# Kernel optimization log

Measured on AMD Instinct MI355X. Metric: run time of the kernel, lower is better.

Reference implementation:

```python
import jax, jax.numpy as jnp
import numpy as np

H_S = 1024
N_HEADS = 16
P_S = H_S // N_HEADS
LN_EPS = 1e-5


def layer_norm(x, gamma, beta):
    mu = jnp.mean(x, axis=-1, keepdims=True)
    var = jnp.var(x, axis=-1, keepdims=True)
    return (x - mu) * jax.lax.rsqrt(var + LN_EPS) * gamma + beta


def setup_inputs() -> dict:
    key = jax.random.key(0)
    ks = jax.random.split(key, 8)
    scale = 1.0 / np.sqrt(H_S)
    B, S = 4, 2048
    return {
        "q": jax.random.normal(ks[0], (B, S, H_S), jnp.float32),
        "k": jax.random.normal(ks[1], (B, S, H_S), jnp.float32),
        "v": jax.random.normal(ks[2], (B, S, H_S), jnp.float32),
        "ln_q_g": jnp.ones((H_S,), jnp.float32),
        "ln_q_b": jnp.zeros((H_S,), jnp.float32),
        "ln_k_g": jnp.ones((H_S,), jnp.float32),
        "ln_k_b": jnp.zeros((H_S,), jnp.float32),
        "ln_v_g": jnp.ones((H_S,), jnp.float32),
        "ln_v_b": jnp.zeros((H_S,), jnp.float32),
        "w_q": jax.random.normal(ks[3], (H_S, H_S), jnp.float32) * scale,
        "w_k": jax.random.normal(ks[4], (H_S, H_S), jnp.float32) * scale,
        "w_v": jax.random.normal(ks[5], (H_S, H_S), jnp.float32) * scale,
        "w_fc": jax.random.normal(ks[6], (H_S, H_S), jnp.float32) * scale,
        "b_fc": jnp.zeros((H_S,), jnp.float32),
    }


def _split_heads(x):
    # (b, s, h_s) -> (b, n_heads, s, p_s)
    b, s, _ = x.shape
    return x.reshape(b, s, N_HEADS, P_S).transpose(0, 2, 1, 3)


def reference(q, k, v, ln_q_g, ln_q_b, ln_k_g, ln_k_b, ln_v_g, ln_v_b,
              w_q, w_k, w_v, w_fc, b_fc):
    b, q_l, _ = q.shape
    # LayerNorm + Linear (bias=False) for Q/K/V, then head split
    qh = _split_heads(layer_norm(q, ln_q_g, ln_q_b) @ w_q.T)
    kh = _split_heads(layer_norm(k, ln_k_g, ln_k_b) @ w_k.T)
    vh = _split_heads(layer_norm(v, ln_v_g, ln_v_b) @ w_v.T)
    # scaled dot-product attention (clipping_distance=None path), scale 1/sqrt(p_s)
    scores = jnp.einsum("bhqp,bhkp->bhqk", qh, kh) / jnp.sqrt(jnp.float32(P_S))
    attn = jax.nn.softmax(scores, axis=-1)
    ctx = jnp.einsum("bhqk,bhkp->bhqp", attn, vh)
    # join heads: (b, h, q, p) -> (b, q, h_s)
    ctx = ctx.transpose(0, 2, 1, 3).reshape(b, q_l, H_S)
    out = ctx @ w_fc.T + b_fc
    # residual (dropout p=0.0 -> identity)
    return q + out
```

## Files before the change

kernel.cpp:

```cpp
#include <hip/hip_runtime.h>

#define HS 1024
#define NH 16
#define PS 64
#define SS 2048
#define NB 4
#define MTOT (NB * SS)
#define QSCALE 0.18033688011112042f

typedef __bf16 bf16x8 __attribute__((ext_vector_type(8)));
typedef float f32x4 __attribute__((ext_vector_type(4)));

__device__ __forceinline__ unsigned short f2bf(float f) {
  union { __bf16 h; unsigned short u; } c;
  c.h = (__bf16)f;
  return c.u;
}
__device__ __forceinline__ unsigned int pk2(float a, float b) {
  union { __bf16 h[2]; unsigned int u; } c;
  c.h[0] = (__bf16)a; c.h[1] = (__bf16)b;
  return c.u;
}
__device__ __forceinline__ float exp2x(float x) {
  float r; asm("v_exp_f32 %0, %1" : "=v"(r) : "v"(x)); return r;
}
__device__ __forceinline__ int kp32(int k) {
  return (k & ~31) | ((k & 12) << 1) | ((k & 16) >> 2) | (k & 3);
}

__device__ __forceinline__ void gload16(const void* g, void* lds) {
  __builtin_amdgcn_global_load_lds(
      (const __attribute__((address_space(1))) unsigned int*)g,
      (__attribute__((address_space(3))) unsigned int*)lds, 16, 0, 0);
}

__device__ __forceinline__ bf16x8 ldfrag128(const unsigned short* base, int r, int c) {
  union { bf16x8 v; uint4 u; } f;
  f.u = *reinterpret_cast<const uint4*>(base + r * 64 + ((c ^ (r & 7)) << 3));
  return f.v;
}

__global__ __launch_bounds__(256) void ln3_kernel(
    const float* __restrict__ x0, const float* __restrict__ x1, const float* __restrict__ x2,
    const float* __restrict__ g0, const float* __restrict__ b0,
    const float* __restrict__ g1, const float* __restrict__ b1,
    const float* __restrict__ g2, const float* __restrict__ b2,
    unsigned short* __restrict__ y0, unsigned short* __restrict__ y1,
    unsigned short* __restrict__ y2) {
  const int z = blockIdx.y;
  const float* x = z == 0 ? x0 : z == 1 ? x1 : x2;
  const float* g = z == 0 ? g0 : z == 1 ? g1 : g2;
  const float* bt = z == 0 ? b0 : z == 1 ? b1 : b2;
  unsigned short* y = z == 0 ? y0 : z == 1 ? y1 : y2;
  const int row = blockIdx.x;
  const int t = threadIdx.x;
  const float4 v = reinterpret_cast<const float4*>(x + (size_t)row * HS)[t];
  float s = v.x + v.y + v.z + v.w;
  float s2 = v.x * v.x + v.y * v.y + v.z * v.z + v.w * v.w;
#pragma unroll
  for (int m = 32; m; m >>= 1) { s += __shfl_xor(s, m); s2 += __shfl_xor(s2, m); }
  __shared__ float red[8];
  if ((t & 63) == 0) { red[t >> 6] = s; red[4 + (t >> 6)] = s2; }
  __syncthreads();
  s = red[0] + red[1] + red[2] + red[3];
  s2 = red[4] + red[5] + red[6] + red[7];
  const float mean = s * (1.0f / HS);
  const float var = s2 * (1.0f / HS) - mean * mean;
  const float rs = rsqrtf(var + 1e-5f);
  const float4 gv = reinterpret_cast<const float4*>(g)[t];
  const float4 bv = reinterpret_cast<const float4*>(bt)[t];
  uint2 o;
  o.x = pk2((v.x - mean) * rs * gv.x + bv.x, (v.y - mean) * rs * gv.y + bv.y);
  o.y = pk2((v.z - mean) * rs * gv.z + bv.z, (v.w - mean) * rs * gv.w + bv.w);
  *reinterpret_cast<uint2*>(y + (size_t)row * HS + kp32(4 * t)) = o;
}

__global__ __launch_bounds__(256) void castw_kernel(
    const float* __restrict__ w0, const float* __restrict__ w1,
    const float* __restrict__ w2, const float* __restrict__ w3,
    unsigned short* __restrict__ o0, unsigned short* __restrict__ o1,
    unsigned short* __restrict__ o2, unsigned short* __restrict__ o3) {
  const int which = blockIdx.x >> 10;
  const float* w = which == 0 ? w0 : which == 1 ? w1 : which == 2 ? w2 : w3;
  unsigned short* o = which == 0 ? o0 : which == 1 ? o1 : which == 2 ? o2 : o3;
  const int i = (blockIdx.x & 1023) * 256 + threadIdx.x;
  float4 v = reinterpret_cast<const float4*>(w)[i];
  uint2 u;
  u.x = pk2(v.x, v.y);
  u.y = pk2(v.z, v.w);
  *reinterpret_cast<uint2*>(o + (size_t)(i >> 8) * 1024 + kp32((i << 2) & 1023)) = u;
}

__global__ __launch_bounds__(512, 4) void gemm_qkv(
    const unsigned short* __restrict__ Aq, const unsigned short* __restrict__ Ak,
    const unsigned short* __restrict__ Av, const unsigned short* __restrict__ Wq,
    const unsigned short* __restrict__ Wk, const unsigned short* __restrict__ Wv,
    unsigned short* __restrict__ Pq, unsigned short* __restrict__ Pk,
    unsigned short* __restrict__ Pv, int zbase) {
  const int z = zbase + blockIdx.z;
  const unsigned short* A = z == 0 ? Aq : z == 1 ? Ak : Av;
  const unsigned short* Bw = z == 0 ? Wq : z == 1 ? Wk : Wv;
  unsigned short* out = z == 0 ? Pq : z == 1 ? Pk : Pv;
  __shared__ unsigned short As[128 * 64];
  __shared__ unsigned short Bs[128 * 64];
  const int t = threadIdx.x;
  const int id = blockIdx.x + 8 * blockIdx.y;
  const int xcd = id & 7, j = id >> 3;
  const int colT = (j & 7) * 128;
  const int rowT = (xcd * 8 + (j >> 3)) * 128;
  const int lane = t & 63;
  const int w = t >> 6;
  const int wr = (w >> 2) * 64, wc = (w & 3) * 32;
  const int c16 = lane & 15, g = lane >> 4, g4 = g << 2;
  const unsigned short* Ab = A + (size_t)rowT * 1024;
  const unsigned short* Bb = Bw + (size_t)colT * 1024;
  f32x4 acc[4][2] = {};
  for (int kt = 0; kt < 1024; kt += 64) {
#pragma unroll
    for (int i = 0; i < 2; ++i) {
      const int c = i * 512 + t;
      const int col = kt + (((c ^ (c >> 3)) & 7) << 3);
      gload16(Ab + (size_t)(c >> 3) * 1024 + col, As + c * 8);
      gload16(Bb + (size_t)(c >> 3) * 1024 + col, Bs + c * 8);
    }
    __syncthreads();
#pragma unroll
    for (int kk = 0; kk < 2; ++kk) {
      bf16x8 aF[4], bF[2];
#pragma unroll
      for (int m = 0; m < 4; ++m) aF[m] = ldfrag128(As, wr + m * 16 + c16, kk * 4 + g);
#pragma unroll
      for (int n = 0; n < 2; ++n) bF[n] = ldfrag128(Bs, wc + n * 16 + c16, kk * 4 + g);
      __builtin_amdgcn_s_setprio(1);
#pragma unroll
      for (int m = 0; m < 4; ++m)
#pragma unroll
        for (int n = 0; n < 2; ++n)
          acc[m][n] = __builtin_amdgcn_mfma_f32_16x16x32_bf16(aF[m], bF[n], acc[m][n], 0, 0, 0);
      __builtin_amdgcn_s_setprio(0);
    }
    __syncthreads();
  }
  const float sc = (z == 0) ? QSCALE : 1.0f;
#pragma unroll
  for (int m = 0; m < 4; ++m) {
#pragma unroll
    for (int n = 0; n < 2; ++n) {
#pragma unroll
      for (int r = 0; r < 4; ++r) {
        const int row = rowT + wr + m * 16 + g4 + r;
        const int col = colT + wc + n * 16 + c16;
        const float val = acc[m][n][r] * sc;
        const int b = row >> 11, s = row & 2047, h = col >> 6, p = col & 63;
        if (z == 2) {
          out[(((size_t)(b * NH + h)) * PS + p) * SS + kp32(s)] = f2bf(val);
        } else {
          out[(((size_t)(b * NH + h)) * SS + s) * PS + kp32(p)] = f2bf(val);
        }
      }
    }
  }
}

__global__ __launch_bounds__(512, 4) void gemm_fc(
    const unsigned short* __restrict__ A, const unsigned short* __restrict__ Bw,
    float* __restrict__ out, const float* __restrict__ resid,
    const float* __restrict__ bias) {
  __shared__ unsigned short As[128 * 64];
  __shared__ unsigned short Bs[128 * 64];
  const int t = threadIdx.x;
  const int id = blockIdx.x + 8 * blockIdx.y;
  const int xcd = id & 7, j = id >> 3;
  const int colT = (j & 7) * 128;
  const int rowT = (xcd * 8 + (j >> 3)) * 128;
  const int lane = t & 63;
  const int w = t >> 6;
  const int wr = (w >> 2) * 64, wc = (w & 3) * 32;
  const int c16 = lane & 15, g = lane >> 4, g4 = g << 2;
  const unsigned short* Ab = A + (size_t)rowT * 1024;
  const unsigned short* Bb = Bw + (size_t)colT * 1024;
  f32x4 acc[4][2] = {};
  for (int kt = 0; kt < 1024; kt += 64) {
#pragma unroll
    for (int i = 0; i < 2; ++i) {
      const int c = i * 512 + t;
      const int col = kt + (((c ^ (c >> 3)) & 7) << 3);
      gload16(Ab + (size_t)(c >> 3) * 1024 + col, As + c * 8);
      gload16(Bb + (size_t)(c >> 3) * 1024 + col, Bs + c * 8);
    }
    __syncthreads();
#pragma unroll
    for (int kk = 0; kk < 2; ++kk) {
      bf16x8 aF[4], bF[2];
#pragma unroll
      for (int m = 0; m < 4; ++m) aF[m] = ldfrag128(As, wr + m * 16 + c16, kk * 4 + g);
#pragma unroll
      for (int n = 0; n < 2; ++n) bF[n] = ldfrag128(Bs, wc + n * 16 + c16, kk * 4 + g);
      __builtin_amdgcn_s_setprio(1);
#pragma unroll
      for (int m = 0; m < 4; ++m)
#pragma unroll
        for (int n = 0; n < 2; ++n)
          acc[m][n] = __builtin_amdgcn_mfma_f32_16x16x32_bf16(aF[m], bF[n], acc[m][n], 0, 0, 0);
      __builtin_amdgcn_s_setprio(0);
    }
    __syncthreads();
  }
#pragma unroll
  for (int m = 0; m < 4; ++m) {
#pragma unroll
    for (int n = 0; n < 2; ++n) {
#pragma unroll
      for (int r = 0; r < 4; ++r) {
        const int row = rowT + wr + m * 16 + g4 + r;
        const int col = colT + wc + n * 16 + c16;
        out[(size_t)row * HS + col] =
            acc[m][n][r] + bias[col] + resid[(size_t)row * HS + col];
      }
    }
  }
}

__device__ __forceinline__ void stage_kv(const unsigned short* Kb, const unsigned short* Vb,
                                         int tile, unsigned short* kd, unsigned short* vd,
                                         int t) {
  const int r = t >> 3;
  const int cc = ((t ^ r) & 7) << 3;
  gload16(Kb + (size_t)(tile * 64 + r) * PS + cc, kd + t * 8);
  gload16(Vb + (size_t)r * SS + tile * 64 + cc, vd + t * 8);
}

__global__ __launch_bounds__(512, 4) void attn_kernel(
    const unsigned short* __restrict__ Qp, const unsigned short* __restrict__ Kp,
    const unsigned short* __restrict__ Vtg, unsigned short* __restrict__ ctx) {
  __shared__ unsigned short Ks[3][64 * 64];
  __shared__ unsigned short Vs[3][64 * 64];
  const int t = threadIdx.x;
  const int w = t >> 6, lane = t & 63;
  const int c16 = lane & 15, g = lane >> 4, g4 = g << 2;
  const int id = blockIdx.x + 8 * blockIdx.y;
  const int xcd = id & 7, j = id >> 3;
  const int bh = xcd * 8 + (j >> 3);
  const int qbase = (j & 7) * 256 + w * 32;
  const unsigned short* Qb = Qp + (size_t)bh * SS * PS;
  const unsigned short* Kb = Kp + (size_t)bh * SS * PS;
  const unsigned short* Vb = Vtg + (size_t)bh * SS * PS;

  union { bf16x8 v; unsigned short s[8]; } ou;
#pragma unroll
  for (int i = 0; i < 8; ++i) ou.s[i] = 0x3F80;
  const bf16x8 onesv = ou.v;

  bf16x8 qF0[2], qF1[2];
#pragma unroll
  for (int kkc = 0; kkc < 2; ++kkc) {
    union { bf16x8 v; uint4 u; } f0, f1;
    f0.u = *reinterpret_cast<const uint4*>(Qb + (size_t)(qbase + c16) * PS + ((kkc * 4 + g) << 3));
    f1.u = *reinterpret_cast<const uint4*>(Qb + (size_t)(qbase + 16 + c16) * PS + ((kkc * 4 + g) << 3));
    qF0[kkc] = f0.v; qF1[kkc] = f1.v;
  }
  f32x4 o0[4] = {}, o1[4] = {};
  f32x4 ol0 = {}, ol1 = {};

  unsigned short *k0 = Ks[0], *k1 = Ks[1], *k2 = Ks[2];
  unsigned short *v0 = Vs[0], *v1 = Vs[1], *v2 = Vs[2];
  stage_kv(Kb, Vb, 0, k0, v0, t);
  stage_kv(Kb, Vb, 1, k1, v1, t);

  for (int kt = 0; kt < 32; ++kt) {
    if (kt < 30) {
      asm volatile("s_waitcnt vmcnt(2) lgkmcnt(0)" ::: "memory");
    } else {
      asm volatile("s_waitcnt vmcnt(0) lgkmcnt(0)" ::: "memory");
    }
    __builtin_amdgcn_s_barrier();
    __builtin_amdgcn_sched_barrier(0);
    if (kt + 2 < 32) stage_kv(Kb, Vb, kt + 2, k2, v2, t);

    f32x4 s0[4] = {}, s1[4] = {};
    __builtin_amdgcn_s_setprio(1);
#pragma unroll
    for (int kkc = 0; kkc < 2; ++kkc)
#pragma unroll
      for (int nf = 0; nf < 4; ++nf) {
        const bf16x8 kf = ldfrag128(k0, nf * 16 + c16, kkc * 4 + g);
        s0[nf] = __builtin_amdgcn_mfma_f32_16x16x32_bf16(kf, qF0[kkc], s0[nf], 0, 0, 0);
        s1[nf] = __builtin_amdgcn_mfma_f32_16x16x32_bf16(kf, qF1[kkc], s1[nf], 0, 0, 0);
      }
    __builtin_amdgcn_s_setprio(0);

#pragma unroll
    for (int nf = 0; nf < 4; ++nf)
#pragma unroll
      for (int r = 0; r < 4; ++r) {
        s0[nf][r] = exp2x(s0[nf][r]);
        s1[nf][r] = exp2x(s1[nf][r]);
      }

    __builtin_amdgcn_s_setprio(1);
#pragma unroll
    for (int kkc = 0; kkc < 2; ++kkc) {
      union { bf16x8 v; unsigned int u[4]; } pa0, pa1;
      pa0.u[0] = pk2(s0[2 * kkc][0], s0[2 * kkc][1]);
      pa0.u[1] = pk2(s0[2 * kkc][2], s0[2 * kkc][3]);
      pa0.u[2] = pk2(s0[2 * kkc + 1][0], s0[2 * kkc + 1][1]);
      pa0.u[3] = pk2(s0[2 * kkc + 1][2], s0[2 * kkc + 1][3]);
      pa1.u[0] = pk2(s1[2 * kkc][0], s1[2 * kkc][1]);
      pa1.u[1] = pk2(s1[2 * kkc][2], s1[2 * kkc][3]);
      pa1.u[2] = pk2(s1[2 * kkc + 1][0], s1[2 * kkc + 1][1]);
      pa1.u[3] = pk2(s1[2 * kkc + 1][2], s1[2 * kkc + 1][3]);
      ol0 = __builtin_amdgcn_mfma_f32_16x16x32_bf16(pa0.v, onesv, ol0, 0, 0, 0);
      ol1 = __builtin_amdgcn_mfma_f32_16x16x32_bf16(pa1.v, onesv, ol1, 0, 0, 0);
#pragma unroll
      for (int pf = 0; pf < 4; ++pf) {
        const bf16x8 vf = ldfrag128(v0, pf * 16 + c16, kkc * 4 + g);
        o0[pf] = __builtin_amdgcn_mfma_f32_16x16x32_bf16(pa0.v, vf, o0[pf], 0, 0, 0);
        o1[pf] = __builtin_amdgcn_mfma_f32_16x16x32_bf16(pa1.v, vf, o1[pf], 0, 0, 0);
      }
    }
    __builtin_amdgcn_s_setprio(0);

    unsigned short* tk = k0; k0 = k1; k1 = k2; k2 = tk;
    unsigned short* tv = v0; v0 = v1; v1 = v2; v2 = tv;
  }

  float i0[4], i1[4];
#pragma unroll
  for (int r = 0; r < 4; ++r) { i0[r] = 1.0f / ol0[r]; i1[r] = 1.0f / ol1[r]; }
  const int b = bh >> 4, h = bh & 15;
#pragma unroll
  for (int pf = 0; pf < 4; ++pf) {
#pragma unroll
    for (int r = 0; r < 4; ++r) {
      const int col = kp32(h * PS + pf * 16 + c16);
      const int sA = qbase + g4 + r, sB = qbase + 16 + g4 + r;
      ctx[((size_t)(b * SS + sA)) * HS + col] = f2bf(o0[pf][r] * i0[r]);
      ctx[((size_t)(b * SS + sB)) * HS + col] = f2bf(o1[pf][r] * i1[r]);
    }
  }
}

extern "C" void kernel_launch(void* const* d_in, const int* in_sizes, int n_in,
                              void* d_out, int out_size, void* d_ws, size_t ws_size,
                              hipStream_t stream) {
  const float* q = (const float*)d_in[0];
  const float* k = (const float*)d_in[1];
  const float* v = (const float*)d_in[2];
  const float* ln_q_g = (const float*)d_in[3];
  const float* ln_q_b = (const float*)d_in[4];
  const float* ln_k_g = (const float*)d_in[5];
  const float* ln_k_b = (const float*)d_in[6];
  const float* ln_v_g = (const float*)d_in[7];
  const float* ln_v_b = (const float*)d_in[8];
  const float* w_q = (const float*)d_in[9];
  const float* w_k = (const float*)d_in[10];
  const float* w_v = (const float*)d_in[11];
  const float* w_fc = (const float*)d_in[12];
  const float* b_fc = (const float*)d_in[13];

  char* ws = (char*)d_ws;
  const bool merged = ws_size >= ((size_t)104 << 20);

  if (merged) {
    unsigned short* xq = (unsigned short*)(ws);
    unsigned short* xk = (unsigned short*)(ws + (16 << 20));
    unsigned short* xv = (unsigned short*)(ws + (32 << 20));
    unsigned short* ctx = (unsigned short*)(ws);
    unsigned short* wqb = (unsigned short*)(ws + (48 << 20));
    unsigned short* wkb = (unsigned short*)(ws + (50 << 20));
    unsigned short* wvb = (unsigned short*)(ws + (52 << 20));
    unsigned short* wfcb = (unsigned short*)(ws + (54 << 20));
    unsigned short* pq = (unsigned short*)(ws + (56 << 20));
    unsigned short* pk = (unsigned short*)(ws + (72 << 20));
    unsigned short* pv = (unsigned short*)(ws + (88 << 20));

    castw_kernel<<<4096, 256, 0, stream>>>(w_q, w_k, w_v, w_fc, wqb, wkb, wvb, wfcb);
    ln3_kernel<<<dim3(MTOT, 3), 256, 0, stream>>>(q, k, v, ln_q_g, ln_q_b, ln_k_g,
                                                  ln_k_b, ln_v_g, ln_v_b, xq, xk, xv);
    gemm_qkv<<<dim3(8, 64, 3), 512, 0, stream>>>(xq, xk, xv, wqb, wkb, wvb, pq, pk, pv, 0);
    attn_kernel<<<dim3(8, 64), 512, 0, stream>>>(pq, pk, pv, ctx);
    gemm_fc<<<dim3(8, 64), 512, 0, stream>>>(ctx, wfcb, (float*)d_out, q, b_fc);
  } else {
    unsigned short* xln = (unsigned short*)(ws);
    unsigned short* ctx = (unsigned short*)(ws);
    unsigned short* wqb = (unsigned short*)(ws + (16 << 20));
    unsigned short* wkb = (unsigned short*)(ws + (18 << 20));
    unsigned short* wvb = (unsigned short*)(ws + (20 << 20));
    unsigned short* wfcb = (unsigned short*)(ws + (22 << 20));
    unsigned short* pq = (unsigned short*)(ws + (24 << 20));
    unsigned short* pk = (unsigned short*)(ws + (40 << 20));
    unsigned short* pv = (unsigned short*)(ws + (56 << 20));

    castw_kernel<<<4096, 256, 0, stream>>>(w_q, w_k, w_v, w_fc, wqb, wkb, wvb, wfcb);
    ln3_kernel<<<dim3(MTOT, 1), 256, 0, stream>>>(q, q, q, ln_q_g, ln_q_b, ln_q_g,
                                                  ln_q_b, ln_q_g, ln_q_b, xln, xln, xln);
    gemm_qkv<<<dim3(8, 64, 1), 512, 0, stream>>>(xln, xln, xln, wqb, wqb, wqb,
                                                 pq, pq, pq, 0);
    ln3_kernel<<<dim3(MTOT, 1), 256, 0, stream>>>(k, k, k, ln_k_g, ln_k_b, ln_k_g,
                                                  ln_k_b, ln_k_g, ln_k_b, xln, xln, xln);
    gemm_qkv<<<dim3(8, 64, 1), 512, 0, stream>>>(xln, xln, xln, wkb, wkb, wkb,
                                                 pk, pk, pk, 1);
    ln3_kernel<<<dim3(MTOT, 1), 256, 0, stream>>>(v, v, v, ln_v_g, ln_v_b, ln_v_g,
                                                  ln_v_b, ln_v_g, ln_v_b, xln, xln, xln);
    gemm_qkv<<<dim3(8, 64, 1), 512, 0, stream>>>(xln, xln, xln, wvb, wvb, wvb,
                                                 pv, pv, pv, 2);
    attn_kernel<<<dim3(8, 64), 512, 0, stream>>>(pq, pk, pv, ctx);
    gemm_fc<<<dim3(8, 64), 512, 0, stream>>>(ctx, wfcb, (float*)d_out, q, b_fc);
  }
}
```

Baseline: 204.5 us.

## Switch attention KV staging to 128-key double-buffered tiles

Replaces the triple-buffered 64-key K/V pipeline with a double-buffered pipeline that stages 128 keys per step, and processes each staged tile as two 64-key halves. This halves the number of barriers and waitcnt synchronisations per block. In exchange the prefetch distance drops from two tiles to one, each step waits for all outstanding loads (vmcnt(0)), and LDS use grows from 48KB to 64KB per block, which may limit occupancy.

After: 201.1 us. No clear change (-1.6%).

```diff
diff --git a/kernel.cpp b/kernel.cpp
--- a/kernel.cpp
+++ b/kernel.cpp
@@ -221,20 +221,28 @@
   }
 }
 
-__device__ __forceinline__ void stage_kv(const unsigned short* Kb, const unsigned short* Vb,
-                                         int tile, unsigned short* kd, unsigned short* vd,
-                                         int t) {
-  const int r = t >> 3;
-  const int cc = ((t ^ r) & 7) << 3;
-  gload16(Kb + (size_t)(tile * 64 + r) * PS + cc, kd + t * 8);
-  gload16(Vb + (size_t)r * SS + tile * 64 + cc, vd + t * 8);
+__device__ __forceinline__ void stage_kv128(const unsigned short* Kb,
+                                            const unsigned short* Vb, int tile,
+                                            unsigned short* kd, unsigned short* vd,
+                                            int t) {
+#pragma unroll
+  for (int i = 0; i < 2; ++i) {
+    const int c = i * 512 + t;
+    const int rk = c >> 3;
+    const int ck = ((c ^ rk) & 7) << 3;
+    gload16(Kb + (size_t)(tile * 128 + rk) * PS + ck, kd + c * 8);
+    const int cc = c & 511;
+    const int rv = cc >> 3;
+    const int cv = ((cc ^ rv) & 7) << 3;
+    gload16(Vb + (size_t)rv * SS + tile * 128 + i * 64 + cv, vd + c * 8);
+  }
 }
 
 __global__ __launch_bounds__(512, 4) void attn_kernel(
     const unsigned short* __restrict__ Qp, const unsigned short* __restrict__ Kp,
     const unsigned short* __restrict__ Vtg, unsigned short* __restrict__ ctx) {
-  __shared__ unsigned short Ks[3][64 * 64];
-  __shared__ unsigned short Vs[3][64 * 64];
+  __shared__ unsigned short Ks[2][128 * 64];
+  __shared__ unsigned short Vs[2][128 * 64];
   const int t = threadIdx.x;
   const int w = t >> 6, lane = t & 63;
   const int c16 = lane & 15, g = lane >> 4, g4 = g << 2;
@@ -262,66 +270,65 @@
   f32x4 o0[4] = {}, o1[4] = {};
   f32x4 ol0 = {}, ol1 = {};
 
-  unsigned short *k0 = Ks[0], *k1 = Ks[1], *k2 = Ks[2];
-  unsigned short *v0 = Vs[0], *v1 = Vs[1], *v2 = Vs[2];
-  stage_kv(Kb, Vb, 0, k0, v0, t);
-  stage_kv(Kb, Vb, 1, k1, v1, t);
-
-  for (int kt = 0; kt < 32; ++kt) {
-    if (kt < 30) {
-      asm volatile("s_waitcnt vmcnt(2) lgkmcnt(0)" ::: "memory");
-    } else {
-      asm volatile("s_waitcnt vmcnt(0) lgkmcnt(0)" ::: "memory");
-    }
+  stage_kv128(Kb, Vb, 0, Ks[0], Vs[0], t);
+
+  int buf = 0;
+  for (int kt = 0; kt < 16; ++kt) {
+    asm volatile("s_waitcnt vmcnt(0) lgkmcnt(0)" ::: "memory");
     __builtin_amdgcn_s_barrier();
     __builtin_amdgcn_sched_barrier(0);
-    if (kt + 2 < 32) stage_kv(Kb, Vb, kt + 2, k2, v2, t);
-
-    f32x4 s0[4] = {}, s1[4] = {};
-    __builtin_amdgcn_s_setprio(1);
-#pragma unroll
-    for (int kkc = 0; kkc < 2; ++kkc)
-#pragma unroll
-      for (int nf = 0; nf < 4; ++nf) {
-        const bf16x8 kf = ldfrag128(k0, nf * 16 + c16, kkc * 4 + g);
-        s0[nf] = __builtin_amdgcn_mfma_f32_16x16x32_bf16(kf, qF0[kkc], s0[nf], 0, 0, 0);
-        s1[nf] = __builtin_amdgcn_mfma_f32_16x16x32_bf16(kf, qF1[kkc], s1[nf], 0, 0, 0);
+    if (kt + 1 < 16) stage_kv128(Kb, Vb, kt + 1, Ks[buf ^ 1], Vs[buf ^ 1], t);
+
+#pragma unroll
+    for (int hh = 0; hh < 2; ++hh) {
+      const unsigned short* kh = &Ks[buf][hh * 4096];
+      const unsigned short* vh = &Vs[buf][hh * 4096];
+
+      f32x4 s0[4] = {}, s1[4] = {};
+      __builtin_amdgcn_s_setprio(1);
+#pragma unroll
+      for (int kkc = 0; kkc < 2; ++kkc)
+#pragma unroll
+        for (int nf = 0; nf < 4; ++nf) {
+          const bf16x8 kf = ldfrag128(kh, nf * 16 + c16, kkc * 4 + g);
+          s0[nf] = __builtin_amdgcn_mfma_f32_16x16x32_bf16(kf, qF0[kkc], s0[nf], 0, 0, 0);
+          s1[nf] = __builtin_amdgcn_mfma_f32_16x16x32_bf16(kf, qF1[kkc], s1[nf], 0, 0, 0);
+        }
+      __builtin_amdgcn_s_setprio(0);
+
+#pragma unroll
+      for (int nf = 0; nf < 4; ++nf)
+#pragma unroll
+        for (int r = 0; r < 4; ++r) {
+          s0[nf][r] = exp2x(s0[nf][r]);
+          s1[nf][r] = exp2x(s1[nf][r]);
+        }
+
+      __builtin_amdgcn_s_setprio(1);
+#pragma unroll
+      for (int kkc = 0; kkc < 2; ++kkc) {
+        union { bf16x8 v; unsigned int u[4]; } pa0, pa1;
+        pa0.u[0] = pk2(s0[2 * kkc][0], s0[2 * kkc][1]);
+        pa0.u[1] = pk2(s0[2 * kkc][2], s0[2 * kkc][3]);
+        pa0.u[2] = pk2(s0[2 * kkc + 1][0], s0[2 * kkc + 1][1]);
+        pa0.u[3] = pk2(s0[2 * kkc + 1][2], s0[2 * kkc + 1][3]);
+        pa1.u[0] = pk2(s1[2 * kkc][0], s1[2 * kkc][1]);
+        pa1.u[1] = pk2(s1[2 * kkc][2], s1[2 * kkc][3]);
+        pa1.u[2] = pk2(s1[2 * kkc + 1][0], s1[2 * kkc + 1][1]);
+        pa1.u[3] = pk2(s1[2 * kkc + 1][2], s1[2 * kkc + 1][3]);
+        ol0 = __builtin_amdgcn_mfma_f32_16x16x32_bf16(pa0.v, onesv, ol0, 0, 0, 0);
+        ol1 = __builtin_amdgcn_mfma_f32_16x16x32_bf16(pa1.v, onesv, ol1, 0, 0, 0);
+#pragma unroll
+        for (int pf = 0; pf < 4; ++pf) {
+          const bf16x8 vf = ldfrag128(vh, pf * 16 + c16, kkc * 4 + g);
+          o0[pf] = __builtin_amdgcn_mfma_f32_16x16x32_bf16(pa0.v, vf, o0[pf], 0, 0, 0);
+          o1[pf] = __builtin_amdgcn_mfma_f32_16x16x32_bf16(pa1.v, vf, o1[pf], 0, 0, 0);
+        }
       }
-    __builtin_amdgcn_s_setprio(0);
-
-#pragma unroll
-    for (int nf = 0; nf < 4; ++nf)
-#pragma unroll
-      for (int r = 0; r < 4; ++r) {
-        s0[nf][r] = exp2x(s0[nf][r]);
-        s1[nf][r] = exp2x(s1[nf][r]);
-      }
-
-    __builtin_amdgcn_s_setprio(1);
-#pragma unroll
-    for (int kkc = 0; kkc < 2; ++kkc) {
-      union { bf16x8 v; unsigned int u[4]; } pa0, pa1;
-      pa0.u[0] = pk2(s0[2 * kkc][0], s0[2 * kkc][1]);
-      pa0.u[1] = pk2(s0[2 * kkc][2], s0[2 * kkc][3]);
-      pa0.u[2] = pk2(s0[2 * kkc + 1][0], s0[2 * kkc + 1][1]);
-      pa0.u[3] = pk2(s0[2 * kkc + 1][2], s0[2 * kkc + 1][3]);
-      pa1.u[0] = pk2(s1[2 * kkc][0], s1[2 * kkc][1]);
-      pa1.u[1] = pk2(s1[2 * kkc][2], s1[2 * kkc][3]);
-      pa1.u[2] = pk2(s1[2 * kkc + 1][0], s1[2 * kkc + 1][1]);
-      pa1.u[3] = pk2(s1[2 * kkc + 1][2], s1[2 * kkc + 1][3]);
-      ol0 = __builtin_amdgcn_mfma_f32_16x16x32_bf16(pa0.v, onesv, ol0, 0, 0, 0);
-      ol1 = __builtin_amdgcn_mfma_f32_16x16x32_bf16(pa1.v, onesv, ol1, 0, 0, 0);
-#pragma unroll
-      for (int pf = 0; pf < 4; ++pf) {
-        const bf16x8 vf = ldfrag128(v0, pf * 16 + c16, kkc * 4 + g);
-        o0[pf] = __builtin_amdgcn_mfma_f32_16x16x32_bf16(pa0.v, vf, o0[pf], 0, 0, 0);
-        o1[pf] = __builtin_amdgcn_mfma_f32_16x16x32_bf16(pa1.v, vf, o1[pf], 0, 0, 0);
-      }
-    }
-    __builtin_amdgcn_s_setprio(0);
-
-    unsigned short* tk = k0; k0 = k1; k1 = k2; k2 = tk;
-    unsigned short* tv = v0; v0 = v1; v1 = v2; v2 = tv;
+      __builtin_amdgcn_s_setprio(0);
+    }
+
+    buf ^= 1;
   }
 
   float i0[4], i1[4];
```
